# Optimization experiments

Measured on AMD Instinct MI355X. Metric: run time of the kernel, lower is better.

Reference implementation:

```python
import jax, jax.numpy as jnp
import numpy as np

T, B, E, F = 2048, 8, 512, 2
N = E * F  # state dim = emb_dim * exp_factor


def setup_inputs() -> dict:
    key = jax.random.key(0)
    ks = jax.random.split(key, 14)
    x = jax.random.normal(ks[0], (T, B, E), dtype=jnp.float32)
    # in/out projections (torch Linear: y = x @ W.T + b; we store W already transposed)
    W_in = jax.random.normal(ks[1], (E, N), dtype=jnp.float32) / np.sqrt(E)
    b_in = jnp.zeros((N,), dtype=jnp.float32)
    W_out = jax.random.normal(ks[2], (N, E), dtype=jnp.float32) / np.sqrt(N)
    b_out = jnp.zeros((E,), dtype=jnp.float32)
    # LRU eigenvalue parameterization (r_min=0, r_max=1)
    u1 = jax.random.uniform(ks[3], (N,), dtype=jnp.float32, minval=1e-4, maxval=1.0)
    u2 = jax.random.uniform(ks[4], (N,), dtype=jnp.float32)
    nu_log = jnp.log(-0.5 * jnp.log(u1))
    theta_log = jnp.log(u2 * 2.0 * np.pi)
    gamma_log = jnp.log(jnp.sqrt(1.0 - jnp.exp(-jnp.exp(nu_log)) ** 2))
    B_real = jax.random.normal(ks[5], (N, N), dtype=jnp.float32) / np.sqrt(2 * E)
    B_imag = jax.random.normal(ks[6], (N, N), dtype=jnp.float32) / np.sqrt(2 * N)
    C_real = jax.random.normal(ks[7], (N, N), dtype=jnp.float32) / np.sqrt(N)
    C_imag = jax.random.normal(ks[8], (N, N), dtype=jnp.float32) / np.sqrt(N)
    D = jax.random.normal(ks[9], (N,), dtype=jnp.float32)
    return {"x": x, "W_in": W_in, "b_in": b_in, "W_out": W_out, "b_out": b_out,
            "nu_log": nu_log, "theta_log": theta_log, "gamma_log": gamma_log,
            "B_real": B_real, "B_imag": B_imag, "C_real": C_real, "C_imag": C_imag,
            "D": D}


def _bin_op(el1, el2):
    a_i, bu_i = el1
    a_j, bu_j = el2
    return (a_j * a_i, a_j * bu_i + bu_j)


def reference(x, W_in, b_in, W_out, b_out, nu_log, theta_log, gamma_log,
              B_real, B_imag, C_real, C_imag, D):
    u = x @ W_in + b_in                                   # [T,B,N] real
    Lam = jnp.exp(-jnp.exp(nu_log) + 1j * jnp.exp(theta_log))        # [N] complex
    B_norm = (B_real + 1j * B_imag) * jnp.exp(gamma_log)[:, None]    # [N,N]
    C = C_real + 1j * C_imag                                          # [N,N]
    # Bu[t,b,j] = sum_i B_norm[i,j] * u[t,b,i]  (matches einsum 'ij,kmi->kmj')
    Bu = jnp.einsum('ij,tbi->tbj', B_norm, u.astype(B_norm.dtype))   # [T,B,N]
    Lam_elems = jnp.broadcast_to(Lam, Bu.shape)                       # [T,B,N]
    # linear recurrence h_t = Lam * h_{t-1} + Bu_t via associative scan over time (axis 0)
    _, h = jax.lax.associative_scan(_bin_op, (Lam_elems, Bu), axis=0)
    y = (jnp.einsum('ij,tbi->tbj', C, h) + D * u).real                # [T,B,N]
    return y @ W_out + b_out                                          # [T,B,E]
```

## Files before the change

kernel.cpp:

```cpp
#include <hip/hip_runtime.h>
#include <hip/hip_bf16.h>

typedef __hip_bfloat16 bf16;
typedef __attribute__((ext_vector_type(8))) short bf16x8;
typedef __attribute__((ext_vector_type(4))) float f32x4;

#define T_DIM 2048
#define B_DIM 8
#define E_DIM 512
#define N_DIM 1024
#define M_ROWS (T_DIM * B_DIM)
#define NCHUNK 64
#define CLEN (T_DIM / NCHUNK)

__device__ __forceinline__ void gload16(const void* g, void* l) {
    __builtin_amdgcn_global_load_lds((const void __attribute__((address_space(1)))*)g,
                                     (void __attribute__((address_space(3)))*)l, 16, 0, 0);
}

__global__ void k_prep(const float* __restrict__ nu_log, const float* __restrict__ theta_log,
                       const float* __restrict__ gamma_log,
                       float* __restrict__ LamR, float* __restrict__ LamI, float* __restrict__ g) {
    int i = blockIdx.x * 256 + threadIdx.x;
    if (i < N_DIM) {
        float nu  = expf(nu_log[i]);
        float th  = expf(theta_log[i]);
        float mag = expf(-nu);
        LamR[i] = mag * cosf(th);
        LamI[i] = mag * sinf(th);
        g[i] = expf(gamma_log[i]);
    }
}

struct __align__(8) bf4 { bf16 v[4]; };
__global__ void k_conv(const float* __restrict__ in, bf16* __restrict__ out, int n4, float mul) {
    int i = blockIdx.x * 256 + threadIdx.x;
    int stride = gridDim.x * 256;
    for (; i < n4; i += stride) {
        float4 v = ((const float4*)in)[i];
        bf4 o;
        o.v[0] = __float2bfloat16(v.x * mul);
        o.v[1] = __float2bfloat16(v.y * mul);
        o.v[2] = __float2bfloat16(v.z * mul);
        o.v[3] = __float2bfloat16(v.w * mul);
        ((bf4*)out)[i] = o;
    }
}

__global__ void k_transpose(const float* __restrict__ in, bf16* __restrict__ out,
                            const float* __restrict__ scale, int R, int C) {
    __shared__ float tile[32][33];
    int tx = threadIdx.x & 31, ty = threadIdx.x >> 5;
    int r0 = blockIdx.y * 32, c0 = blockIdx.x * 32;
#pragma unroll
    for (int i = 0; i < 32; i += 8) {
        int r = r0 + ty + i;
        float v = in[(size_t)r * C + c0 + tx];
        if (scale) v *= scale[r];
        tile[ty + i][tx] = v;
    }
    __syncthreads();
#pragma unroll
    for (int i = 0; i < 32; i += 8) {
        out[(size_t)(c0 + ty + i) * R + r0 + tx] = __float2bfloat16(tile[tx][ty + i]);
    }
}

__global__ void k_bias_bu(const float* __restrict__ b_in, const float* __restrict__ g,
                          const float* __restrict__ B_real, const float* __restrict__ B_imag,
                          float* __restrict__ c_bu) {
    int id = blockIdx.x;
    int jblk = id & 7, ic = id >> 3;
    int j = jblk * 256 + threadIdx.x;
    const float* B = (j < N_DIM) ? B_real : B_imag;
    int jj = j & (N_DIM - 1);
    float s = 0.f;
    for (int i = ic * 128; i < ic * 128 + 128; ++i)
        s = fmaf(b_in[i] * g[i], B[(size_t)i * N_DIM + jj], s);
    atomicAdd(&c_bu[j], s);
}

__global__ void k_bias_out(const float* __restrict__ b_out, const float* __restrict__ b_in,
                           const float* __restrict__ D, const float* __restrict__ W_out,
                           float* __restrict__ bo) {
    int id = blockIdx.x;
    int eblk = id & 1, ic = id >> 1;
    int e = eblk * 256 + threadIdx.x;
    float s = (ic == 0) ? b_out[e] : 0.f;
    for (int j = ic * 128; j < ic * 128 + 128; ++j)
        s = fmaf(b_in[j] * D[j], W_out[(size_t)j * E_DIM + e], s);
    atomicAdd(&bo[e], s);
}

template <bool BIAS>
__device__ __forceinline__ void gemm128_core(bf16* lA, bf16* lB,
        const bf16* __restrict__ A, int lda, const bf16* __restrict__ Bt, int ldb,
        bf16* __restrict__ outp, int ldo, const float* __restrict__ bias, int K,
        int bn, int bm) {
    const int tid = threadIdx.x;
    const int lane = tid & 63, w = tid >> 6;
    const int wr = w >> 1, wc = w & 1;
    const int fr = lane & 15, fq = lane >> 4;
    f32x4 acc[4][4] = {};
    for (int k0 = 0; k0 < K; k0 += 32) {
#pragma unroll
        for (int L = 0; L < 2; ++L) {
            int idx = L * 256 + tid;
            int rr = idx >> 2, kk = (idx & 3) * 8;
            gload16(A + (size_t)(bm * 128 + rr) * lda + k0 + kk, lA + idx * 8);
            gload16(Bt + (size_t)(bn * 128 + rr) * ldb + k0 + kk, lB + idx * 8);
        }
        __syncthreads();
        bf16x8 af[4], bfr[4];
#pragma unroll
        for (int i = 0; i < 4; ++i)
            af[i] = *(const bf16x8*)(lA + (wr * 64 + i * 16 + fr) * 32 + fq * 8);
#pragma unroll
        for (int i = 0; i < 4; ++i)
            bfr[i] = *(const bf16x8*)(lB + (wc * 64 + i * 16 + fr) * 32 + fq * 8);
#pragma unroll
        for (int i = 0; i < 4; ++i)
#pragma unroll
            for (int j = 0; j < 4; ++j)
                acc[i][j] = __builtin_amdgcn_mfma_f32_16x16x32_bf16(af[i], bfr[j], acc[i][j], 0, 0, 0);
        __syncthreads();
    }
    const int orow = bm * 128 + wr * 64;
    const int ocol = bn * 128 + wc * 64;
#pragma unroll
    for (int i = 0; i < 4; ++i)
#pragma unroll
        for (int j = 0; j < 4; ++j) {
            int col = ocol + j * 16 + fr;
            float bv = BIAS ? bias[col] : 0.0f;
#pragma unroll
            for (int r = 0; r < 4; ++r) {
                int row = orow + i * 16 + fq * 4 + r;
                outp[(size_t)row * ldo + col] = __float2bfloat16(acc[i][j][r] + bv);
            }
        }
}

__global__ __launch_bounds__(256)
void k_g1(const bf16* __restrict__ xb, const bf16* __restrict__ WBcat,
          bf16* __restrict__ BuH, const float* __restrict__ c_bu) {
    __shared__ __align__(16) bf16 lA[128 * 32];
    __shared__ __align__(16) bf16 lB[128 * 32];
    int id = blockIdx.x;
    int swz = (id & 7) * 256 + (id >> 3);
    int bn = swz & 15, bm = swz >> 4;
    gemm128_core<true>(lA, lB, xb, 512, WBcat, 512, BuH, 2048, c_bu, 512, bn, bm);
}

__global__ __launch_bounds__(256)
void k_gemm4(const bf16* __restrict__ BscT, const bf16* __restrict__ Win_b,
             const bf16* __restrict__ WoT, const bf16* __restrict__ WoTD,
             const bf16* __restrict__ Cr_b, const bf16* __restrict__ Ci_b,
             bf16* __restrict__ WBcat, bf16* __restrict__ Bfin) {
    __shared__ __align__(16) bf16 lA[128 * 32];
    __shared__ __align__(16) bf16 lB[128 * 32];
    int id = blockIdx.x;
    if (id < 64) {
        gemm128_core<false>(lA, lB, BscT, 1024, Win_b, 1024, WBcat, 512, nullptr, 1024, id & 3, id >> 2);
    } else if (id < 96) {
        int l = id - 64;
        gemm128_core<false>(lA, lB, WoT, 1024, Cr_b, 1024, Bfin, 2560, nullptr, 1024, l & 7, l >> 3);
    } else if (id < 128) {
        int l = id - 96;
        gemm128_core<false>(lA, lB, WoT, 1024, Ci_b, 1024, Bfin + 1024, 2560, nullptr, 1024, l & 7, l >> 3);
    } else {
        int l = id - 128;
        gemm128_core<false>(lA, lB, WoTD, 1024, Win_b, 1024, Bfin + 2048, 2560, nullptr, 1024, l & 3, l >> 2);
    }
}

template <bool ASPLIT>
__global__ __launch_bounds__(256, 1)
void k_gemm_wn(const bf16* __restrict__ A0, const bf16* __restrict__ A1, int ksplit,
               int lda0, int lda1, const bf16* __restrict__ Bt, int ldb,
               float* __restrict__ outp, int ldo, const float* __restrict__ bias, int K) {
    __shared__ __align__(16) bf16 lA[2][64 * 32];
    __shared__ __align__(16) bf16 lB[2][512 * 32];
    const int tid = threadIdx.x;
    const int bm = blockIdx.x;
    const int lane = tid & 63, w = tid >> 6;
    const int fr = lane & 15, fq = lane >> 4;
    f32x4 acc[4][8] = {};
    const int nt = K / 32;

    auto stage = [&](int buf, int t) {
        int k0 = t * 32;
        const bf16* Ap = A0; int lda = lda0, ac = k0;
        if (ASPLIT && k0 >= ksplit) { Ap = A1; lda = lda1; ac = k0 - ksplit; }
        {
            int rr = tid >> 2, s = tid & 3;
            int kk = (s ^ (rr & 3)) * 8;
            gload16(Ap + (size_t)(bm * 64 + rr) * lda + ac + kk, &lA[buf][tid * 8]);
        }
#pragma unroll
        for (int L = 0; L < 8; ++L) {
            int idx = L * 256 + tid;
            int rr = idx >> 2, s = idx & 3;
            int kk = (s ^ (rr & 3)) * 8;
            gload16(Bt + (size_t)rr * ldb + k0 + kk, &lB[buf][idx * 8]);
        }
    };

    stage(0, 0);
    __syncthreads();
    int cur = 0;
    for (int t = 0; t < nt; ++t) {
        if (t + 1 < nt) stage(cur ^ 1, t + 1);
        bf16x8 af[4], bfr[8];
#pragma unroll
        for (int i = 0; i < 4; ++i) {
            int rr = i * 16 + fr;
            af[i] = *(const bf16x8*)(&lA[cur][(rr * 4 + (fq ^ (rr & 3))) * 8]);
        }
#pragma unroll
        for (int j = 0; j < 8; ++j) {
            int rr = w * 128 + j * 16 + fr;
            bfr[j] = *(const bf16x8*)(&lB[cur][(rr * 4 + (fq ^ (rr & 3))) * 8]);
        }
#pragma unroll
        for (int i = 0; i < 4; ++i)
#pragma unroll
            for (int j = 0; j < 8; ++j)
                acc[i][j] = __builtin_amdgcn_mfma_f32_16x16x32_bf16(af[i], bfr[j], acc[i][j], 0, 0, 0);
        __syncthreads();
        cur ^= 1;
    }
    const int orow = bm * 64;
#pragma unroll
    for (int i = 0; i < 4; ++i)
#pragma unroll
        for (int j = 0; j < 8; ++j) {
            int col = w * 128 + j * 16 + fr;
            float bv = bias[col];
#pragma unroll
            for (int r = 0; r < 4; ++r)
                outp[(size_t)(orow + i * 16 + fq * 4 + r) * ldo + col] = acc[i][j][r] + bv;
        }
}

__global__ void k_scan_carry(const bf16* __restrict__ BuH, const float* __restrict__ LamR,
                             const float* __restrict__ LamI, float2* __restrict__ carry) {
    int tid = blockIdx.x * 256 + threadIdx.x;
    int n = tid & (N_DIM - 1);
    int bb = (tid >> 10) & 7;
    int c = tid >> 13;
    float lr = LamR[n], li = LamI[n];
    float hr = 0.f, hi = 0.f;
    const bf16* p = BuH + ((size_t)(c * CLEN) * B_DIM + bb) * 2048 + n;
#pragma unroll 8
    for (int t = 0; t < CLEN; ++t) {
        float br = __bfloat162float(p[0]);
        float bi = __bfloat162float(p[N_DIM]);
        float nr = fmaf(lr, hr, fmaf(-li, hi, br));
        float ni = fmaf(lr, hi, fmaf(li, hr, bi));
        hr = nr; hi = ni;
        p += B_DIM * 2048;
    }
    carry[tid] = make_float2(hr, hi);
}

__global__ void k_scan_combine(const float2* __restrict__ carry, float2* __restrict__ S,
                               const float* __restrict__ LamR, const float* __restrict__ LamI) {
    int tid = blockIdx.x * 256 + threadIdx.x;
    int n = tid & (N_DIM - 1);
    float ar = LamR[n], ai = LamI[n];
#pragma unroll
    for (int s = 0; s < 5; ++s) { float nr = ar * ar - ai * ai, ni = 2.f * ar * ai; ar = nr; ai = ni; }
    float sr = 0.f, si = 0.f;
    for (int c = 0; c < NCHUNK; ++c) {
        S[(size_t)c * 8192 + tid] = make_float2(sr, si);
        float2 ca = carry[(size_t)c * 8192 + tid];
        float nr = fmaf(ar, sr, fmaf(-ai, si, ca.x));
        float ni = fmaf(ar, si, fmaf(ai, sr, ca.y));
        sr = nr; si = ni;
    }
}

__global__ void k_scan_apply(bf16* __restrict__ BuH, const float* __restrict__ LamR,
                             const float* __restrict__ LamI, const float2* __restrict__ S) {
    int tid = blockIdx.x * 256 + threadIdx.x;
    int n = tid & (N_DIM - 1);
    int bb = (tid >> 10) & 7;
    int c = tid >> 13;
    float lr = LamR[n], li = LamI[n];
    float2 s0 = S[tid];
    float hr = s0.x, hi = s0.y;
    bf16* p = BuH + ((size_t)(c * CLEN) * B_DIM + bb) * 2048 + n;
#pragma unroll 8
    for (int t = 0; t < CLEN; ++t) {
        float br = __bfloat162float(p[0]);
        float bi = __bfloat162float(p[N_DIM]);
        float nr = fmaf(lr, hr, fmaf(-li, hi, br));
        float ni = fmaf(lr, hi, fmaf(li, hr, bi));
        hr = nr; hi = ni;
        p[0] = __float2bfloat16(hr);
        p[N_DIM] = __float2bfloat16(hi);
        p += B_DIM * 2048;
    }
}

extern "C" void kernel_launch(void* const* d_in, const int* in_sizes, int n_in,
                              void* d_out, int out_size, void* d_ws, size_t ws_size,
                              hipStream_t stream) {
    const float* x         = (const float*)d_in[0];
    const float* W_in      = (const float*)d_in[1];
    const float* b_in      = (const float*)d_in[2];
    const float* W_out     = (const float*)d_in[3];
    const float* b_out     = (const float*)d_in[4];
    const float* nu_log    = (const float*)d_in[5];
    const float* theta_log = (const float*)d_in[6];
    const float* gamma_log = (const float*)d_in[7];
    const float* B_real    = (const float*)d_in[8];
    const float* B_imag    = (const float*)d_in[9];
    const float* C_real    = (const float*)d_in[10];
    const float* C_imag    = (const float*)d_in[11];
    const float* Dvec      = (const float*)d_in[12];
    float* out = (float*)d_out;

    char* ws = (char*)d_ws;
    size_t off = 0;
    auto alloc = [&](size_t bytes) { void* p = ws + off; off = (off + bytes + 255) & ~(size_t)255; return p; };
    bf16*  xb    = (bf16*)alloc((size_t)M_ROWS * E_DIM * 2);
    bf16*  BuH   = (bf16*)alloc((size_t)M_ROWS * 2048 * 2);
    bf16*  BscT  = (bf16*)alloc((size_t)2048 * 1024 * 2);
    bf16*  Win_b = (bf16*)alloc((size_t)512 * 1024 * 2);
    bf16*  Cr_b  = (bf16*)alloc((size_t)1024 * 1024 * 2);
    bf16*  Ci_b  = (bf16*)alloc((size_t)1024 * 1024 * 2);
    bf16*  WoT   = (bf16*)alloc((size_t)512 * 1024 * 2);
    bf16*  WoTD  = (bf16*)alloc((size_t)512 * 1024 * 2);
    bf16*  WBcat = (bf16*)alloc((size_t)2048 * 512 * 2);
    bf16*  Bfin  = (bf16*)alloc((size_t)512 * 2560 * 2);
    float* LamR  = (float*)alloc(1024 * 4);
    float* LamI  = (float*)alloc(1024 * 4);
    float* gvec  = (float*)alloc(1024 * 4);
    float* c_bu  = (float*)alloc(2048 * 4);
    float* biasO = (float*)alloc(512 * 4);
    float2* carry = (float2*)alloc((size_t)NCHUNK * 8192 * 8);
    float2* Sbuf  = (float2*)alloc((size_t)NCHUNK * 8192 * 8);

    k_prep<<<4, 256, 0, stream>>>(nu_log, theta_log, gamma_log, LamR, LamI, gvec);
    k_conv<<<2048, 256, 0, stream>>>(x, xb, M_ROWS * E_DIM / 4, 1.f);
    k_conv<<<512, 256, 0, stream>>>(W_in, Win_b, 512 * 1024 / 4, 1.f);
    k_conv<<<1024, 256, 0, stream>>>(C_real, Cr_b, 1024 * 1024 / 4, 1.f);
    k_conv<<<1024, 256, 0, stream>>>(C_imag, Ci_b, 1024 * 1024 / 4, -1.f);
    k_transpose<<<dim3(32, 32), 256, 0, stream>>>(B_real, BscT, gvec, 1024, 1024);
    k_transpose<<<dim3(32, 32), 256, 0, stream>>>(B_imag, BscT + (size_t)1024 * 1024, gvec, 1024, 1024);
    k_transpose<<<dim3(16, 32), 256, 0, stream>>>(W_out, WoT, nullptr, 1024, 512);
    k_transpose<<<dim3(16, 32), 256, 0, stream>>>(W_out, WoTD, Dvec, 1024, 512);

    hipMemsetAsync(c_bu, 0, 2048 * 4, stream);
    hipMemsetAsync(biasO, 0, 512 * 4, stream);
    k_bias_bu<<<64, 256, 0, stream>>>(b_in, gvec, B_real, B_imag, c_bu);
    k_bias_out<<<16, 256, 0, stream>>>(b_out, b_in, Dvec, W_out, biasO);

    k_gemm4<<<144, 256, 0, stream>>>(BscT, Win_b, WoT, WoTD, Cr_b, Ci_b, WBcat, Bfin);

    k_g1<<<2048, 256, 0, stream>>>(xb, WBcat, BuH, c_bu);

    k_scan_carry<<<NCHUNK * 8192 / 256, 256, 0, stream>>>(BuH, LamR, LamI, carry);
    k_scan_combine<<<32, 256, 0, stream>>>(carry, Sbuf, LamR, LamI);
    k_scan_apply<<<NCHUNK * 8192 / 256, 256, 0, stream>>>(BuH, LamR, LamI, Sbuf);

    k_gemm_wn<true><<<256, 256, 0, stream>>>(BuH, xb, 2048, 2048, 512, Bfin, 2560, out, 512, biasO, 2560);
}
```

Baseline: 412.4 us.

## Batch conversion/transpose launches and double-buffer all GEMMs with swizzled LDS

Merges the four fp32->bf16 conversion launches into one kernel and the four transpose launches into another, which cuts launch overhead. Replaces the single-buffered 128x128 GEMM core with a double-buffered version that XOR-swizzles the LDS layout and raises wave priority around the MFMA block. This core is used for the first GEMM, the weight-prep GEMMs, and a new final GEMM. The final GEMM moves from 256 blocks of 64x512 tiles to 512 blocks of 128x128 tiles with a block swizzle. The trade is doubled LDS per block, which may lower occupancy, and smaller N tiles that reload more A data in the final GEMM.

```diff
diff --git a/kernel.cpp b/kernel.cpp
--- a/kernel.cpp
+++ b/kernel.cpp
@@ -33,25 +33,40 @@
 }
 
 struct __align__(8) bf4 { bf16 v[4]; };
-__global__ void k_conv(const float* __restrict__ in, bf16* __restrict__ out, int n4, float mul) {
-    int i = blockIdx.x * 256 + threadIdx.x;
-    int stride = gridDim.x * 256;
-    for (; i < n4; i += stride) {
-        float4 v = ((const float4*)in)[i];
-        bf4 o;
-        o.v[0] = __float2bfloat16(v.x * mul);
-        o.v[1] = __float2bfloat16(v.y * mul);
-        o.v[2] = __float2bfloat16(v.z * mul);
-        o.v[3] = __float2bfloat16(v.w * mul);
-        ((bf4*)out)[i] = o;
-    }
-}
-
-__global__ void k_transpose(const float* __restrict__ in, bf16* __restrict__ out,
-                            const float* __restrict__ scale, int R, int C) {
+__global__ void k_conv_all(const float* __restrict__ x, const float* __restrict__ W_in,
+                           const float* __restrict__ C_r, const float* __restrict__ C_i,
+                           bf16* __restrict__ xb, bf16* __restrict__ Win_b,
+                           bf16* __restrict__ Cr_b, bf16* __restrict__ Ci_b) {
+    int id = blockIdx.x;
+    const float* src; bf16* dst; float mul = 1.f; int base;
+    if (id < 8192)      { src = x;    dst = xb;    base = id; }
+    else if (id < 8704) { src = W_in; dst = Win_b; base = id - 8192; }
+    else if (id < 9728) { src = C_r;  dst = Cr_b;  base = id - 8704; }
+    else                { src = C_i;  dst = Ci_b;  base = id - 9728; mul = -1.f; }
+    int i = base * 256 + threadIdx.x;
+    float4 v = ((const float4*)src)[i];
+    bf4 o;
+    o.v[0] = __float2bfloat16(v.x * mul);
+    o.v[1] = __float2bfloat16(v.y * mul);
+    o.v[2] = __float2bfloat16(v.z * mul);
+    o.v[3] = __float2bfloat16(v.w * mul);
+    ((bf4*)dst)[i] = o;
+}
+
+__global__ void k_transpose_all(const float* __restrict__ B_r, const float* __restrict__ B_i,
+                                const float* __restrict__ W_out, const float* __restrict__ gvec,
+                                const float* __restrict__ Dvec,
+                                bf16* __restrict__ BscT, bf16* __restrict__ WoT,
+                                bf16* __restrict__ WoTD) {
     __shared__ float tile[32][33];
+    int id = blockIdx.x;
+    const float* in; bf16* out; const float* scale; int R, C, bx, by;
+    if (id < 1024)      { in = B_r;   out = BscT;                      scale = gvec; R = 1024; C = 1024; bx = id & 31;          by = id >> 5; }
+    else if (id < 2048) { int l = id - 1024; in = B_i; out = BscT + (size_t)1024 * 1024; scale = gvec; R = 1024; C = 1024; bx = l & 31; by = l >> 5; }
+    else if (id < 2560) { int l = id - 2048; in = W_out; out = WoT;    scale = nullptr; R = 1024; C = 512; bx = l & 15; by = l >> 4; }
+    else                { int l = id - 2560; in = W_out; out = WoTD;   scale = Dvec;   R = 1024; C = 512; bx = l & 15; by = l >> 4; }
     int tx = threadIdx.x & 31, ty = threadIdx.x >> 5;
-    int r0 = blockIdx.y * 32, c0 = blockIdx.x * 32;
+    int r0 = by * 32, c0 = bx * 32;
 #pragma unroll
     for (int i = 0; i < 32; i += 8) {
         int r = r0 + ty + i;
@@ -92,38 +107,61 @@
     atomicAdd(&bo[e], s);
 }
 
-template <bool BIAS>
-__device__ __forceinline__ void gemm128_core(bf16* lA, bf16* lB,
-        const bf16* __restrict__ A, int lda, const bf16* __restrict__ Bt, int ldb,
-        bf16* __restrict__ outp, int ldo, const float* __restrict__ bias, int K,
+template <bool ASPLIT, bool OUTF32, bool BIAS>
+__device__ __forceinline__ void gemm_db_core(bf16* lds,
+        const bf16* __restrict__ A0, const bf16* __restrict__ A1, int ksplit,
+        int lda0, int lda1, const bf16* __restrict__ Bt, int ldb,
+        void* __restrict__ outp, int ldo, const float* __restrict__ bias, int K,
         int bn, int bm) {
     const int tid = threadIdx.x;
     const int lane = tid & 63, w = tid >> 6;
     const int wr = w >> 1, wc = w & 1;
     const int fr = lane & 15, fq = lane >> 4;
     f32x4 acc[4][4] = {};
-    for (int k0 = 0; k0 < K; k0 += 32) {
+    const int nt = K / 32;
+
+    auto stage = [&](int buf, int t) {
+        int k0 = t * 32;
+        const bf16* Ap = A0; int lda = lda0, ac = k0;
+        if (ASPLIT && k0 >= ksplit) { Ap = A1; lda = lda1; ac = k0 - ksplit; }
+        bf16* dst = lds + buf * 8192;
 #pragma unroll
         for (int L = 0; L < 2; ++L) {
             int idx = L * 256 + tid;
-            int rr = idx >> 2, kk = (idx & 3) * 8;
-            gload16(A + (size_t)(bm * 128 + rr) * lda + k0 + kk, lA + idx * 8);
-            gload16(Bt + (size_t)(bn * 128 + rr) * ldb + k0 + kk, lB + idx * 8);
+            int rr = idx >> 2, s = idx & 3;
+            int kk = (s ^ (rr & 3)) * 8;
+            gload16(Ap + (size_t)(bm * 128 + rr) * lda + ac + kk, dst + idx * 8);
+            gload16(Bt + (size_t)(bn * 128 + rr) * ldb + k0 + kk, dst + 4096 + idx * 8);
         }
-        __syncthreads();
+    };
+
+    stage(0, 0);
+    __syncthreads();
+    int cur = 0;
+    for (int t = 0; t < nt; ++t) {
+        if (t + 1 < nt) stage(cur ^ 1, t + 1);
+        const bf16* bufA = lds + cur * 8192;
+        const bf16* bufB = bufA + 4096;
         bf16x8 af[4], bfr[4];
 #pragma unroll
-        for (int i = 0; i < 4; ++i)
-            af[i] = *(const bf16x8*)(lA + (wr * 64 + i * 16 + fr) * 32 + fq * 8);
-#pragma unroll
-        for (int i = 0; i < 4; ++i)
-            bfr[i] = *(const bf16x8*)(lB + (wc * 64 + i * 16 + fr) * 32 + fq * 8);
+        for (int i = 0; i < 4; ++i) {
+            int rr = wr * 64 + i * 16 + fr;
+            af[i] = *(const bf16x8*)(bufA + (rr * 4 + (fq ^ (rr & 3))) * 8);
+        }
+#pragma unroll
+        for (int j = 0; j < 4; ++j) {
+            int rr = wc * 64 + j * 16 + fr;
+            bfr[j] = *(const bf16x8*)(bufB + (rr * 4 + (fq ^ (rr & 3))) * 8);
+        }
+        __builtin_amdgcn_s_setprio(1);
 #pragma unroll
         for (int i = 0; i < 4; ++i)
 #pragma unroll
             for (int j = 0; j < 4; ++j)
                 acc[i][j] = __builtin_amdgcn_mfma_f32_16x16x32_bf16(af[i], bfr[j], acc[i][j], 0, 0, 0);
+        __builtin_amdgcn_s_setprio(0);
         __syncthreads();
+        cur ^= 1;
     }
     const int orow = bm * 128 + wr * 64;
     const int ocol = bn * 128 + wc * 64;
@@ -136,7 +174,9 @@
 #pragma unroll
             for (int r = 0; r < 4; ++r) {
                 int row = orow + i * 16 + fq * 4 + r;
-                outp[(size_t)row * ldo + col] = __float2bfloat16(acc[i][j][r] + bv);
+                float v = acc[i][j][r] + bv;
+                if (OUTF32) ((float*)outp)[(size_t)row * ldo + col] = v;
+                else        ((bf16*)outp)[(size_t)row * ldo + col] = __float2bfloat16(v);
             }
         }
 }
@@ -144,12 +184,24 @@
 __global__ __launch_bounds__(256)
 void k_g1(const bf16* __restrict__ xb, const bf16* __restrict__ WBcat,
           bf16* __restrict__ BuH, const float* __restrict__ c_bu) {
-    __shared__ __align__(16) bf16 lA[128 * 32];
-    __shared__ __align__(16) bf16 lB[128 * 32];
+    __shared__ __align__(16) bf16 lds[2 * 8192];
     int id = blockIdx.x;
     int swz = (id & 7) * 256 + (id >> 3);
     int bn = swz & 15, bm = swz >> 4;
-    gemm128_core<true>(lA, lB, xb, 512, WBcat, 512, BuH, 2048, c_bu, 512, bn, bm);
+    gemm_db_core<false, false, true>(lds, xb, nullptr, 0, 512, 0, WBcat, 512,
+                                     BuH, 2048, c_bu, 512, bn, bm);
+}
+
+__global__ __launch_bounds__(256)
+void k_g2(const bf16* __restrict__ BuH, const bf16* __restrict__ xb,
+          const bf16* __restrict__ Bfin, float* __restrict__ out,
+          const float* __restrict__ biasO) {
+    __shared__ __align__(16) bf16 lds[2 * 8192];
+    int id = blockIdx.x;
+    int swz = (id & 7) * 64 + (id >> 3);
+    int bn = swz & 3, bm = swz >> 2;
+    gemm_db_core<true, true, true>(lds, BuH, xb, 2048, 2048, 512, Bfin, 2560,
+                                   out, 512, biasO, 2560, bn, bm);
 }
 
 __global__ __launch_bounds__(256)
@@ -157,90 +209,20 @@
              const bf16* __restrict__ WoT, const bf16* __restrict__ WoTD,
              const bf16* __restrict__ Cr_b, const bf16* __restrict__ Ci_b,
              bf16* __restrict__ WBcat, bf16* __restrict__ Bfin) {
-    __shared__ __align__(16) bf16 lA[128 * 32];
-    __shared__ __align__(16) bf16 lB[128 * 32];
+    __shared__ __align__(16) bf16 lds[2 * 8192];
     int id = blockIdx.x;
     if (id < 64) {
-        gemm128_core<false>(lA, lB, BscT, 1024, Win_b, 1024, WBcat, 512, nullptr, 1024, id & 3, id >> 2);
+        gemm_db_core<false, false, false>(lds, BscT, nullptr, 0, 1024, 0, Win_b, 1024, WBcat, 512, nullptr, 1024, id & 3, id >> 2);
     } else if (id < 96) {
         int l = id - 64;
-        gemm128_core<false>(lA, lB, WoT, 1024, Cr_b, 1024, Bfin, 2560, nullptr, 1024, l & 7, l >> 3);
+        gemm_db_core<false, false, false>(lds, WoT, nullptr, 0, 1024, 0, Cr_b, 1024, Bfin, 2560, nullptr, 1024, l & 7, l >> 3);
     } else if (id < 128) {
         int l = id - 96;
-        gemm128_core<false>(lA, lB, WoT, 1024, Ci_b, 1024, Bfin + 1024, 2560, nullptr, 1024, l & 7, l >> 3);
+        gemm_db_core<false, false, false>(lds, WoT, nullptr, 0, 1024, 0, Ci_b, 1024, Bfin + 1024, 2560, nullptr, 1024, l & 7, l >> 3);
     } else {
         int l = id - 128;
-        gemm128_core<false>(lA, lB, WoTD, 1024, Win_b, 1024, Bfin + 2048, 2560, nullptr, 1024, l & 3, l >> 2);
-    }
-}
-
-template <bool ASPLIT>
-__global__ __launch_bounds__(256, 1)
-void k_gemm_wn(const bf16* __restrict__ A0, const bf16* __restrict__ A1, int ksplit,
-               int lda0, int lda1, const bf16* __restrict__ Bt, int ldb,
-               float* __restrict__ outp, int ldo, const float* __restrict__ bias, int K) {
-    __shared__ __align__(16) bf16 lA[2][64 * 32];
-    __shared__ __align__(16) bf16 lB[2][512 * 32];
-    const int tid = threadIdx.x;
-    const int bm = blockIdx.x;
-    const int lane = tid & 63, w = tid >> 6;
-    const int fr = lane & 15, fq = lane >> 4;
-    f32x4 acc[4][8] = {};
-    const int nt = K / 32;
-
-    auto stage = [&](int buf, int t) {
-        int k0 = t * 32;
-        const bf16* Ap = A0; int lda = lda0, ac = k0;
-        if (ASPLIT && k0 >= ksplit) { Ap = A1; lda = lda1; ac = k0 - ksplit; }
-        {
-            int rr = tid >> 2, s = tid & 3;
-            int kk = (s ^ (rr & 3)) * 8;
-            gload16(Ap + (size_t)(bm * 64 + rr) * lda + ac + kk, &lA[buf][tid * 8]);
-        }
-#pragma unroll
-        for (int L = 0; L < 8; ++L) {
-            int idx = L * 256 + tid;
-            int rr = idx >> 2, s = idx & 3;
-            int kk = (s ^ (rr & 3)) * 8;
-            gload16(Bt + (size_t)rr * ldb + k0 + kk, &lB[buf][idx * 8]);
-        }
-    };
-
-    stage(0, 0);
-    __syncthreads();
-    int cur = 0;
-    for (int t = 0; t < nt; ++t) {
-        if (t + 1 < nt) stage(cur ^ 1, t + 1);
-        bf16x8 af[4], bfr[8];
-#pragma unroll
-        for (int i = 0; i < 4; ++i) {
-            int rr = i * 16 + fr;
-            af[i] = *(const bf16x8*)(&lA[cur][(rr * 4 + (fq ^ (rr & 3))) * 8]);
-        }
-#pragma unroll
-        for (int j = 0; j < 8; ++j) {
-            int rr = w * 128 + j * 16 + fr;
-            bfr[j] = *(const bf16x8*)(&lB[cur][(rr * 4 + (fq ^ (rr & 3))) * 8]);
-        }
-#pragma unroll
-        for (int i = 0; i < 4; ++i)
-#pragma unroll
-            for (int j = 0; j < 8; ++j)
-                acc[i][j] = __builtin_amdgcn_mfma_f32_16x16x32_bf16(af[i], bfr[j], acc[i][j], 0, 0, 0);
-        __syncthreads();
-        cur ^= 1;
-    }
-    const int orow = bm * 64;
-#pragma unroll
-    for (int i = 0; i < 4; ++i)
-#pragma unroll
-        for (int j = 0; j < 8; ++j) {
-            int col = w * 128 + j * 16 + fr;
-            float bv = bias[col];
-#pragma unroll
-            for (int r = 0; r < 4; ++r)
-                outp[(size_t)(orow + i * 16 + fq * 4 + r) * ldo + col] = acc[i][j][r] + bv;
-        }
+        gemm_db_core<false, false, false>(lds, WoTD, nullptr, 0, 1024, 0, Win_b, 1024, Bfin + 2048, 2560, nullptr, 1024, l & 3, l >> 2);
+    }
 }
 
 __global__ void k_scan_carry(const bf16* __restrict__ BuH, const float* __restrict__ LamR,
@@ -344,14 +326,8 @@
     float2* Sbuf  = (float2*)alloc((size_t)NCHUNK * 8192 * 8);
 
     k_prep<<<4, 256, 0, stream>>>(nu_log, theta_log, gamma_log, LamR, LamI, gvec);
-    k_conv<<<2048, 256, 0, stream>>>(x, xb, M_ROWS * E_DIM / 4, 1.f);
-    k_conv<<<512, 256, 0, stream>>>(W_in, Win_b, 512 * 1024 / 4, 1.f);
-    k_conv<<<1024, 256, 0, stream>>>(C_real, Cr_b, 1024 * 1024 / 4, 1.f);
-    k_conv<<<1024, 256, 0, stream>>>(C_imag, Ci_b, 1024 * 1024 / 4, -1.f);
-    k_transpose<<<dim3(32, 32), 256, 0, stream>>>(B_real, BscT, gvec, 1024, 1024);
-    k_transpose<<<dim3(32, 32), 256, 0, stream>>>(B_imag, BscT + (size_t)1024 * 1024, gvec, 1024, 1024);
-    k_transpose<<<dim3(16, 32), 256, 0, stream>>>(W_out, WoT, nullptr, 1024, 512);
-    k_transpose<<<dim3(16, 32), 256, 0, stream>>>(W_out, WoTD, Dvec, 1024, 512);
+    k_conv_all<<<10752, 256, 0, stream>>>(x, W_in, C_real, C_imag, xb, Win_b, Cr_b, Ci_b);
+    k_transpose_all<<<3072, 256, 0, stream>>>(B_real, B_imag, W_out, gvec, Dvec, BscT, WoT, WoTD);
 
     hipMemsetAsync(c_bu, 0, 2048 * 4, stream);
     hipMemsetAsync(biasO, 0, 512 * 4, stream);
@@ -366,5 +342,5 @@
     k_scan_combine<<<32, 256, 0, stream>>>(carry, Sbuf, LamR, LamI);
     k_scan_apply<<<NCHUNK * 8192 / 256, 256, 0, stream>>>(BuH, LamR, LamI, Sbuf);
 
-    k_gemm_wn<true><<<256, 256, 0, stream>>>(BuH, xb, 2048, 2048, 512, Bfin, 2560, out, 512, biasO, 2560);
-}
+    k_g2<<<512, 256, 0, stream>>>(BuH, xb, Bfin, out, biasO);
+}
```

Measured after the change: 339.2 us. 1.22x faster.
